# Kernel tuning notes

Hardware: AMD Instinct MI355X
Metric: run time of the kernel (lower is better)

The kernel has to match this reference:

```python
import jax, jax.numpy as jnp
import numpy as np

N = 100000      # nodes
E = 800000      # edges
F_IN = 256      # input feature dim
HID = 256       # hidden_channels
H = 8           # heads
C = HID // H    # per-head dim = 32
OUT = 128       # out_channels
EPS_BN = 1e-5
NEG_SLOPE = 0.2


def _segment_softmax(logits, seg, n):
    # logits: [E, H], softmax over edges sharing the same destination node
    m = jax.ops.segment_max(logits, seg, num_segments=n)          # [N, H]
    m = jnp.where(jnp.isfinite(m), m, 0.0)                         # nodes with no in-edges
    ex = jnp.exp(logits - m[seg])                                  # [E, H]
    denom = jax.ops.segment_sum(ex, seg, num_segments=n)          # [N, H]
    return ex / (denom[seg] + 1e-16)


def _gatv2_layer(x, src, dst, Wl, bl, Wr, br, att, bias):
    # PyG GATv2Conv (eval, concat=True): lin_l on source, lin_r on target
    n = x.shape[0]
    xl = (x @ Wl + bl).reshape(n, H, C)   # [N, H, C]
    xr = (x @ Wr + br).reshape(n, H, C)   # [N, H, C]
    e = jax.nn.leaky_relu(xl[src] + xr[dst], NEG_SLOPE)            # [E, H, C]
    logits = jnp.einsum('ehc,hc->eh', e, att)                      # [E, H]
    alpha = _segment_softmax(logits, dst, n)                       # [E, H]
    msg = xl[src] * alpha[:, :, None]                              # [E, H, C]
    out = jax.ops.segment_sum(msg, dst, num_segments=n)            # [N, H, C]
    return out.reshape(n, H * C) + bias


def _batchnorm(x, gamma, beta):
    # training-mode batch statistics (deterministic), biased variance
    mu = x.mean(axis=0)
    var = x.var(axis=0)
    return gamma * (x - mu) * jax.lax.rsqrt(var + EPS_BN) + beta


def setup_inputs() -> dict:
    key = jax.random.key(0)
    ks = jax.random.split(key, 12)
    s = 0.05
    z = jnp.zeros
    o = jnp.ones
    rn = lambda k, shp: jax.random.normal(k, shp, jnp.float32) * s
    return {
        'x': jax.random.normal(ks[0], (N, F_IN), jnp.float32),
        'edge_index': jax.random.randint(ks[1], (2, E), 0, N, jnp.int32),
        'Wl1': rn(ks[2], (F_IN, HID)), 'bl1': z((HID,), jnp.float32),
        'Wr1': rn(ks[3], (F_IN, HID)), 'br1': z((HID,), jnp.float32),
        'att1': rn(ks[4], (H, C)), 'bias1': z((HID,), jnp.float32),
        'gamma1': o((HID,), jnp.float32), 'beta1': z((HID,), jnp.float32),
        'Wl2': rn(ks[5], (HID, HID)), 'bl2': z((HID,), jnp.float32),
        'Wr2': rn(ks[6], (HID, HID)), 'br2': z((HID,), jnp.float32),
        'att2': rn(ks[7], (H, C)), 'bias2': z((HID,), jnp.float32),
        'gamma2': o((HID,), jnp.float32), 'beta2': z((HID,), jnp.float32),
        'Wfc': rn(ks[8], (HID, OUT)), 'bfc': z((OUT,), jnp.float32),
    }


def reference(x, edge_index, Wl1, bl1, Wr1, br1, att1, bias1, gamma1, beta1,
              Wl2, bl2, Wr2, br2, att2, bias2, gamma2, beta2, Wfc, bfc):
    src, dst = edge_index[0], edge_index[1]
    h = _gatv2_layer(x, src, dst, Wl1, bl1, Wr1, br1, att1, bias1)
    h = jax.nn.elu(_batchnorm(h, gamma1, beta1))
    h = _gatv2_layer(h, src, dst, Wl2, bl2, Wr2, br2, att2, bias2)
    h = jax.nn.elu(_batchnorm(h, gamma2, beta2))
    h = h @ Wfc + bfc
    # F.normalize(p=2, dim=-1)
    norm = jnp.maximum(jnp.linalg.norm(h, axis=-1, keepdims=True), 1e-12)
    return h / norm
```

## Files before the change

kernel.cpp:

```cpp
#include <hip/hip_runtime.h>
#include <math.h>

#define N_NODES 100000
#define N_EDGES 800000
#define NPAD    100096
#define FDIM 256
#define HEADS 8
#define CDIM 32
#define OUTF 128

#define SCAN_BLOCK 256
#define SCAN_NBLK ((N_NODES + SCAN_BLOCK - 1) / SCAN_BLOCK)

typedef _Float16 f16x2 __attribute__((ext_vector_type(2)));
typedef _Float16 f16x8 __attribute__((ext_vector_type(8)));
typedef float  f32x4 __attribute__((ext_vector_type(4)));
typedef unsigned short u16;

__device__ __forceinline__ u16 f2h(float f) {
    union { _Float16 h; u16 u; } c;
    c.h = (_Float16)f;
    return c.u;
}
__device__ __forceinline__ float h2f(u16 u) {
    union { u16 u; _Float16 h; } c;
    c.u = u;
    return (float)c.h;
}
__device__ __forceinline__ f16x2 u2h2(unsigned u) {
    return __builtin_bit_cast(f16x2, u);
}
__device__ __forceinline__ unsigned h2u2(f16x2 h) {
    return __builtin_bit_cast(unsigned, h);
}

__device__ __forceinline__ void gload_lds16(const void* g, void* l) {
    __builtin_amdgcn_global_load_lds((const __attribute__((address_space(1))) void*)g,
                                     (__attribute__((address_space(3))) void*)l, 16, 0, 0);
}

__global__ void cast_half(const float* __restrict__ src, int n_valid4, int n_pad4,
                          u16* __restrict__ dst) {
    int i = blockIdx.x * blockDim.x + threadIdx.x;
    int stride = gridDim.x * blockDim.x;
    for (; i < n_pad4; i += stride) {
        f32x4 v = {0.f, 0.f, 0.f, 0.f};
        if (i < n_valid4) v = ((const f32x4*)src)[i];
        ((ushort4*)dst)[i] = make_ushort4(f2h(v[0]), f2h(v[1]), f2h(v[2]), f2h(v[3]));
    }
}

__global__ void prep_w_layer(const float* __restrict__ Wl, const float* __restrict__ Wr,
                             u16* __restrict__ Wt) {
    int idx = blockIdx.x * blockDim.x + threadIdx.x;
    if (idx >= 512 * 256) return;
    int n = idx >> 8, k = idx & 255;
    float w = (n < 256) ? Wl[k * 256 + n] : Wr[k * 256 + (n - 256)];
    Wt[idx] = f2h(w);
}

__global__ void prep_w_fc(const float* __restrict__ Wfc, u16* __restrict__ Wt) {
    int idx = blockIdx.x * blockDim.x + threadIdx.x;
    if (idx >= 128 * 256) return;
    int n = idx >> 8, k = idx & 255;
    Wt[idx] = f2h(Wfc[k * 128 + n]);
}

template <bool HOUT, int NS, bool L2N>
__global__ __launch_bounds__(256) void gemm_h(
        const u16* __restrict__ A, const u16* __restrict__ Wt,
        const float* __restrict__ bias0, const float* __restrict__ bias1,
        void* __restrict__ C0v, void* __restrict__ C1v, int ldc, int M) {
    __shared__ __align__(16) u16 lA[2][128 * 64];
    __shared__ __align__(16) u16 lB[2][128 * 64];
    __shared__ float rssq[128];

    int tid = threadIdx.x;
    int wid = tid >> 6, lane = tid & 63;
    int wm = wid >> 1, wn = wid & 1;
    int lr = lane & 15, lk = lane >> 4;

    int orig = blockIdx.x;
    int nwg = gridDim.x;
    int q = nwg >> 3, r = nwg & 7;
    int xcd = orig & 7, loc = orig >> 3;
    int swz = (xcd < r) ? (xcd * (q + 1) + loc) : (r * (q + 1) + (xcd - r) * q + loc);
    int m0 = (swz / NS) * 128;
    int n0 = (swz % NS) * 128;

    auto stage = [&](int buf, int k0) {
#pragma unroll
        for (int i = 0; i < 4; i++) {
            int t = i * 256 + tid;
            int row = t >> 3;
            int ch = (t & 7) ^ (row & 7);
            gload_lds16(A + (size_t)(m0 + row) * 256 + k0 + ch * 8,
                        (char*)lA[buf] + i * 4096 + wid * 1024);
        }
#pragma unroll
        for (int i = 0; i < 4; i++) {
            int t = i * 256 + tid;
            int row = t >> 3;
            int ch = (t & 7) ^ (row & 7);
            gload_lds16(Wt + (size_t)(n0 + row) * 256 + k0 + ch * 8,
                        (char*)lB[buf] + i * 4096 + wid * 1024);
        }
    };

    f32x4 acc[4][4] = {};

    stage(0, 0);
    __syncthreads();

#pragma unroll 1
    for (int ks = 0; ks < 4; ks++) {
        int cur = ks & 1;
        if (ks < 3) stage(cur ^ 1, (ks + 1) * 64);

#pragma unroll
        for (int kk = 0; kk < 2; kk++) {
            f16x8 af[4], bf[4];
#pragma unroll
            for (int mr = 0; mr < 4; mr++) {
                int rr = wm * 64 + mr * 16 + lr;
                int qq = (kk * 4 + lk) ^ (rr & 7);
                af[mr] = *(const f16x8*)&lA[cur][rr * 64 + qq * 8];
            }
#pragma unroll
            for (int nr = 0; nr < 4; nr++) {
                int rr = wn * 64 + nr * 16 + lr;
                int qq = (kk * 4 + lk) ^ (rr & 7);
                bf[nr] = *(const f16x8*)&lB[cur][rr * 64 + qq * 8];
            }
#pragma unroll
            for (int mr = 0; mr < 4; mr++)
#pragma unroll
                for (int nr = 0; nr < 4; nr++)
                    acc[mr][nr] = __builtin_amdgcn_mfma_f32_16x16x32_f16(
                        af[mr], bf[nr], acc[mr][nr], 0, 0, 0);
        }
        __syncthreads();
    }

#pragma unroll
    for (int mr = 0; mr < 4; mr++)
#pragma unroll
        for (int nr = 0; nr < 4; nr++) {
            int col = n0 + wn * 64 + nr * 16 + lr;
            float b = (col < 256) ? bias0[col] : bias1[col - 256];
#pragma unroll
            for (int j = 0; j < 4; j++) acc[mr][nr][j] += b;
        }

    if constexpr (L2N) {
        if (tid < 128) rssq[tid] = 0.f;
        __syncthreads();
#pragma unroll
        for (int mr = 0; mr < 4; mr++)
#pragma unroll
            for (int j = 0; j < 4; j++) {
                int rl = wm * 64 + mr * 16 + lk * 4 + j;
                float s = 0.f;
#pragma unroll
                for (int nr = 0; nr < 4; nr++) s += acc[mr][nr][j] * acc[mr][nr][j];
                atomicAdd(&rssq[rl], s);
            }
        __syncthreads();
#pragma unroll
        for (int mr = 0; mr < 4; mr++)
#pragma unroll
            for (int j = 0; j < 4; j++) {
                int rl = wm * 64 + mr * 16 + lk * 4 + j;
                int row = m0 + rl;
                if (row < M) {
                    float inv = 1.f / fmaxf(sqrtf(rssq[rl]), 1e-12f);
#pragma unroll
                    for (int nr = 0; nr < 4; nr++) {
                        int col = n0 + wn * 64 + nr * 16 + lr;
                        ((float*)C0v)[(size_t)row * ldc + col] = acc[mr][nr][j] * inv;
                    }
                }
            }
    } else {
#pragma unroll
        for (int mr = 0; mr < 4; mr++)
#pragma unroll
            for (int nr = 0; nr < 4; nr++) {
                int col = n0 + wn * 64 + nr * 16 + lr;
                void* Cp; int c;
                if (col < 256) { Cp = C0v; c = col; }
                else           { Cp = C1v; c = col - 256; }
#pragma unroll
                for (int j = 0; j < 4; j++) {
                    int row = m0 + wm * 64 + mr * 16 + lk * 4 + j;
                    if (row < M) {
                        float v = acc[mr][nr][j];
                        if constexpr (HOUT)
                            ((u16*)Cp)[(size_t)row * ldc + c] = f2h(v);
                        else
                            ((float*)Cp)[(size_t)row * ldc + c] = v;
                    }
                }
            }
    }
}

__global__ void count_deg(const int* __restrict__ dstA, int* __restrict__ deg) {
    int i = blockIdx.x * blockDim.x + threadIdx.x;
    int stride = gridDim.x * blockDim.x;
    for (; i < N_EDGES; i += stride) atomicAdd(&deg[dstA[i]], 1);
}

__global__ void scan_phase1(const int* __restrict__ deg, int* __restrict__ blocksum) {
    __shared__ int sdata[SCAN_BLOCK];
    int i = blockIdx.x * SCAN_BLOCK + threadIdx.x;
    sdata[threadIdx.x] = (i < N_NODES) ? deg[i] : 0;
    __syncthreads();
    for (int off = SCAN_BLOCK / 2; off > 0; off >>= 1) {
        if (threadIdx.x < off) sdata[threadIdx.x] += sdata[threadIdx.x + off];
        __syncthreads();
    }
    if (threadIdx.x == 0) blocksum[blockIdx.x] = sdata[0];
}

__global__ void scan_phase2(int* __restrict__ blocksum) {
    __shared__ int part[512];
    int t = threadIdx.x;
    int v = (t < SCAN_NBLK) ? blocksum[t] : 0;
    part[t] = v;
    __syncthreads();
    for (int off = 1; off < 512; off <<= 1) {
        int u = 0;
        if (t >= off) u = part[t - off];
        __syncthreads();
        if (t >= off) part[t] += u;
        __syncthreads();
    }
    if (t < SCAN_NBLK) blocksum[t] = part[t] - v;
}

__global__ void scan_phase3(const int* __restrict__ deg, const int* __restrict__ blockoff,
                            int* __restrict__ rowstart, int* __restrict__ cursor) {
    __shared__ int part[SCAN_BLOCK];
    int t = threadIdx.x;
    int i = blockIdx.x * SCAN_BLOCK + t;
    int v = (i < N_NODES) ? deg[i] : 0;
    part[t] = v;
    __syncthreads();
    for (int off = 1; off < SCAN_BLOCK; off <<= 1) {
        int u = 0;
        if (t >= off) u = part[t - off];
        __syncthreads();
        if (t >= off) part[t] += u;
        __syncthreads();
    }
    if (i < N_NODES) {
        int excl = blockoff[blockIdx.x] + part[t] - v;
        rowstart[i] = excl;
        cursor[i] = excl;
        if (i == N_NODES - 1) rowstart[N_NODES] = blockoff[blockIdx.x] + part[t];
    }
}

__global__ void fill_csr(const int* __restrict__ srcA, const int* __restrict__ dstA,
                         int* __restrict__ cursor, int* __restrict__ csr_src) {
    int i = blockIdx.x * blockDim.x + threadIdx.x;
    int stride = gridDim.x * blockDim.x;
    for (; i < N_EDGES; i += stride) {
        int pos = atomicAdd(&cursor[dstA[i]], 1);
        csr_src[pos] = srcA[i];
    }
}

__global__ void gat_fused(const u16* __restrict__ xl, const u16* __restrict__ xr,
                          const int* __restrict__ rowstart, const int* __restrict__ csr_src,
                          const float* __restrict__ att, u16* __restrict__ out) {
    int wid = (blockIdx.x * blockDim.x + threadIdx.x) >> 6;
    int lane = threadIdx.x & 63;
    if (wid >= N_NODES) return;
    int hl = lane & 31;
    int up = lane >> 5;
    int c0 = hl * 8;

    uint4 xru = *(const uint4*)(xr + (size_t)wid * FDIM + c0);
    f16x2 xr0 = u2h2(xru.x), xr1 = u2h2(xru.y), xr2 = u2h2(xru.z), xr3 = u2h2(xru.w);
    f32x4 av0 = *(const f32x4*)(att + c0);
    f32x4 av1 = *(const f32x4*)(att + c0 + 4);
    f16x2 a0 = {(_Float16)av0[0], (_Float16)av0[1]};
    f16x2 a1 = {(_Float16)av0[2], (_Float16)av0[3]};
    f16x2 a2 = {(_Float16)av1[0], (_Float16)av1[1]};
    f16x2 a3 = {(_Float16)av1[2], (_Float16)av1[3]};
    const f16x2 k02 = {(_Float16)0.2f, (_Float16)0.2f};

    f16x2 acc0 = {(_Float16)0.f, (_Float16)0.f};
    f16x2 acc1 = acc0, acc2 = acc0, acc3 = acc0;
    float den = 0.f;

    int jb = rowstart[wid], je = rowstart[wid + 1];
    if (jb < je) {
        int jlast = je - 1;
        int nsteps = (je - jb + 1) >> 1;
        int i0 = jb + up;     if (i0 > jlast) i0 = jlast;
        uint4 u0 = *(const uint4*)(xl + (size_t)csr_src[i0] * FDIM + c0);
        int i1 = jb + 2 + up; if (i1 > jlast) i1 = jlast;
        uint4 u1 = *(const uint4*)(xl + (size_t)csr_src[i1] * FDIM + c0);
        int i2 = jb + 4 + up; if (i2 > jlast) i2 = jlast;
        uint4 u2 = *(const uint4*)(xl + (size_t)csr_src[i2] * FDIM + c0);

        for (int t = 0; t < nsteps; ++t) {
            int in_ = jb + 2 * t + 6 + up; if (in_ > jlast) in_ = jlast;
            uint4 un = *(const uint4*)(xl + (size_t)csr_src[in_] * FDIM + c0);

            int myidx = jb + 2 * t + up;
            f16x2 x0 = u2h2(u0.x), x1 = u2h2(u0.y), x2 = u2h2(u0.z), x3 = u2h2(u0.w);
            f16x2 v0 = x0 + xr0, v1 = x1 + xr1, v2 = x2 + xr2, v3 = x3 + xr3;
            f16x2 t0 = __builtin_elementwise_max(v0, v0 * k02);
            f16x2 t1 = __builtin_elementwise_max(v1, v1 * k02);
            f16x2 t2 = __builtin_elementwise_max(v2, v2 * k02);
            f16x2 t3 = __builtin_elementwise_max(v3, v3 * k02);
            float s = __builtin_amdgcn_fdot2(t0, a0, 0.f, false);
            s = __builtin_amdgcn_fdot2(t1, a1, s, false);
            s = __builtin_amdgcn_fdot2(t2, a2, s, false);
            s = __builtin_amdgcn_fdot2(t3, a3, s, false);
            s += __shfl_xor(s, 1);
            s += __shfl_xor(s, 2);
            float e = (myidx <= jlast) ? __expf(s) : 0.f;
            den += e;
            _Float16 eh = (_Float16)e;
            f16x2 ev = {eh, eh};
            acc0 += ev * x0;
            acc1 += ev * x1;
            acc2 += ev * x2;
            acc3 += ev * x3;
            u0 = u1; u1 = u2; u2 = un;
        }
    }
    den += __shfl_xor(den, 32);
    acc0 += u2h2(__shfl_xor((int)h2u2(acc0), 32));
    acc1 += u2h2(__shfl_xor((int)h2u2(acc1), 32));
    acc2 += u2h2(__shfl_xor((int)h2u2(acc2), 32));
    acc3 += u2h2(__shfl_xor((int)h2u2(acc3), 32));

    if (up == 0) {
        float invf = 1.f / (den + 1e-16f);
        u16 h[8];
        h[0] = f2h((float)acc0[0] * invf); h[1] = f2h((float)acc0[1] * invf);
        h[2] = f2h((float)acc1[0] * invf); h[3] = f2h((float)acc1[1] * invf);
        h[4] = f2h((float)acc2[0] * invf); h[5] = f2h((float)acc2[1] * invf);
        h[6] = f2h((float)acc3[0] * invf); h[7] = f2h((float)acc3[1] * invf);
        *(uint4*)(out + (size_t)wid * FDIM + c0) = *(const uint4*)h;
    }
}

__global__ void bn_stats_h(const u16* __restrict__ X, float* __restrict__ sum,
                           float* __restrict__ sumsq, int nrows) {
    int col = threadIdx.x;
    float s = 0.f, ss = 0.f;
    for (int r = blockIdx.x; r < nrows; r += gridDim.x) {
        float v = h2f(X[(size_t)r * FDIM + col]);
        s += v;
        ss += v * v;
    }
    atomicAdd(&sum[col], s);
    atomicAdd(&sumsq[col], ss);
}

__global__ void bn_finalize(const float* __restrict__ sum, const float* __restrict__ sumsq,
                            const float* __restrict__ gamma, const float* __restrict__ beta,
                            float* __restrict__ scale, float* __restrict__ shift) {
    int c = threadIdx.x;
    float mean = sum[c] * (1.f / N_NODES);
    float var = sumsq[c] * (1.f / N_NODES) - mean * mean;
    float sc = gamma[c] * rsqrtf(var + 1e-5f);
    scale[c] = sc;
    shift[c] = beta[c] - mean * sc;
}

__global__ void bn_elu_h(const u16* __restrict__ X, const float* __restrict__ scale,
                         const float* __restrict__ shift, u16* __restrict__ dst) {
    int i = blockIdx.x * blockDim.x + threadIdx.x;
    int stride = gridDim.x * blockDim.x;
    const int n_valid4 = N_NODES * FDIM / 4;
    const int n_pad4 = NPAD * FDIM / 4;
    for (; i < n_pad4; i += stride) {
        u16 h[4] = {0, 0, 0, 0};
        if (i < n_valid4) {
            ushort4 v = ((const ushort4*)X)[i];
            int c0 = (i * 4) & (FDIM - 1);
            float f0 = h2f(v.x) * scale[c0 + 0] + shift[c0 + 0];
            float f1 = h2f(v.y) * scale[c0 + 1] + shift[c0 + 1];
            float f2 = h2f(v.z) * scale[c0 + 2] + shift[c0 + 2];
            float f3 = h2f(v.w) * scale[c0 + 3] + shift[c0 + 3];
            f0 = f0 > 0.f ? f0 : expf(f0) - 1.f;
            f1 = f1 > 0.f ? f1 : expf(f1) - 1.f;
            f2 = f2 > 0.f ? f2 : expf(f2) - 1.f;
            f3 = f3 > 0.f ? f3 : expf(f3) - 1.f;
            h[0] = f2h(f0); h[1] = f2h(f1); h[2] = f2h(f2); h[3] = f2h(f3);
        }
        ((ushort4*)dst)[i] = make_ushort4(h[0], h[1], h[2], h[3]);
    }
}

extern "C" void kernel_launch(void* const* d_in, const int* in_sizes, int n_in,
                              void* d_out, int out_size, void* d_ws, size_t ws_size,
                              hipStream_t stream) {
    const float* x     = (const float*)d_in[0];
    const int*   ei    = (const int*)d_in[1];
    const float* Wl1   = (const float*)d_in[2];
    const float* bl1   = (const float*)d_in[3];
    const float* Wr1   = (const float*)d_in[4];
    const float* br1   = (const float*)d_in[5];
    const float* att1  = (const float*)d_in[6];
    const float* gamma1 = (const float*)d_in[8];
    const float* beta1  = (const float*)d_in[9];
    const float* Wl2   = (const float*)d_in[10];
    const float* bl2   = (const float*)d_in[11];
    const float* Wr2   = (const float*)d_in[12];
    const float* br2   = (const float*)d_in[13];
    const float* att2  = (const float*)d_in[14];
    const float* gamma2 = (const float*)d_in[16];
    const float* beta2  = (const float*)d_in[17];
    const float* Wfc   = (const float*)d_in[18];
    const float* bfc   = (const float*)d_in[19];

    const int* srcA = ei;
    const int* dstA = ei + N_EDGES;

    const size_t REG = (size_t)NPAD * FDIM * 4;
    char* p = (char*)d_ws;
    char* R0 = p;            p += REG;
    char* R1 = p;            p += REG;
    char* R2 = p;            p += REG;
    u16* WTH   = (u16*)p;              p += 512 * 256 * 2;
    float* SUM = (float*)p;            p += FDIM * 4;
    float* SQ  = (float*)p;            p += FDIM * 4;
    float* SC  = (float*)p;            p += FDIM * 4;
    float* SH  = (float*)p;            p += FDIM * 4;
    int* DEG      = (int*)p;           p += (size_t)N_NODES * 4;
    int* ROWSTART = (int*)p;           p += (size_t)(N_NODES + 1) * 4;
    int* CURSOR   = (int*)p;           p += (size_t)N_NODES * 4;
    int* CSR      = (int*)p;           p += (size_t)N_EDGES * 4;
    int* BLKSUM   = (int*)p;           p += (size_t)SCAN_NBLK * 4;

    const int gat_grid = (N_NODES + 3) / 4;
    const int gemm_grid_layer = (NPAD / 128) * 4;
    const int gemm_grid_fc = NPAD / 128;

    hipMemsetAsync(DEG, 0, (size_t)N_NODES * sizeof(int), stream);
    count_deg<<<2048, 256, 0, stream>>>(dstA, DEG);
    scan_phase1<<<SCAN_NBLK, SCAN_BLOCK, 0, stream>>>(DEG, BLKSUM);
    scan_phase2<<<1, 512, 0, stream>>>(BLKSUM);
    scan_phase3<<<SCAN_NBLK, SCAN_BLOCK, 0, stream>>>(DEG, BLKSUM, ROWSTART, CURSOR);
    fill_csr<<<2048, 256, 0, stream>>>(srcA, dstA, CURSOR, CSR);

    cast_half<<<4096, 256, 0, stream>>>(x, N_NODES * FDIM / 4, NPAD * FDIM / 4, (u16*)R0);
    prep_w_layer<<<512, 256, 0, stream>>>(Wl1, Wr1, WTH);
    gemm_h<true, 4, false><<<gemm_grid_layer, 256, 0, stream>>>((u16*)R0, WTH, bl1, br1, R1, R2, 256, N_NODES);
    gat_fused<<<gat_grid, 256, 0, stream>>>((u16*)R1, (u16*)R2, ROWSTART, CSR, att1, (u16*)R0);

    hipMemsetAsync(SUM, 0, 2 * FDIM * sizeof(float), stream);
    bn_stats_h<<<1024, 256, 0, stream>>>((u16*)R0, SUM, SQ, N_NODES);
    bn_finalize<<<1, 256, 0, stream>>>(SUM, SQ, gamma1, beta1, SC, SH);
    bn_elu_h<<<2048, 256, 0, stream>>>((u16*)R0, SC, SH, (u16*)R1);

    prep_w_layer<<<512, 256, 0, stream>>>(Wl2, Wr2, WTH);
    gemm_h<true, 4, false><<<gemm_grid_layer, 256, 0, stream>>>((u16*)R1, WTH, bl2, br2, R2, R0, 256, N_NODES);
    gat_fused<<<gat_grid, 256, 0, stream>>>((u16*)R2, (u16*)R0, ROWSTART, CSR, att2, (u16*)R1);

    hipMemsetAsync(SUM, 0, 2 * FDIM * sizeof(float), stream);
    bn_stats_h<<<1024, 256, 0, stream>>>((u16*)R1, SUM, SQ, N_NODES);
    bn_finalize<<<1, 256, 0, stream>>>(SUM, SQ, gamma2, beta2, SC, SH);
    bn_elu_h<<<2048, 256, 0, stream>>>((u16*)R1, SC, SH, (u16*)R2);

    prep_w_fc<<<128, 256, 0, stream>>>(Wfc, WTH);
    gemm_h<false, 1, true><<<gemm_grid_fc, 256, 0, stream>>>((u16*)R2, WTH, bfc, bfc, d_out, d_out, 128, N_NODES);
}
```

Baseline: 631.8 us.

## Widen GEMM to 8 waves, batch GAT gathers by 8, vectorize BN stats

The GEMM kernel now runs 512 threads per block. Each wave computes a 32x64 sub-tile instead of 64x64, which roughly halves the accumulator registers per thread and puts more waves on each CU. The GAT aggregation loop now handles 8 edges per iteration and issues four gathered row loads ahead of time per lane pair, instead of a rolling 3-deep prefetch, to keep more memory requests in flight. bn_stats reads 4 halves per thread, reduces across the block in shared memory and issues fewer atomics. The costs are more clamped redundant loads for low-degree nodes and a larger block-level sync footprint in the GEMM.

```diff
diff --git a/kernel.cpp b/kernel.cpp
--- a/kernel.cpp
+++ b/kernel.cpp
@@ -67,7 +67,7 @@
 }
 
 template <bool HOUT, int NS, bool L2N>
-__global__ __launch_bounds__(256) void gemm_h(
+__global__ __launch_bounds__(512) void gemm_h(
         const u16* __restrict__ A, const u16* __restrict__ Wt,
         const float* __restrict__ bias0, const float* __restrict__ bias1,
         void* __restrict__ C0v, void* __restrict__ C1v, int ldc, int M) {
@@ -90,24 +90,24 @@
 
     auto stage = [&](int buf, int k0) {
 #pragma unroll
-        for (int i = 0; i < 4; i++) {
-            int t = i * 256 + tid;
+        for (int i = 0; i < 2; i++) {
+            int t = i * 512 + tid;
             int row = t >> 3;
             int ch = (t & 7) ^ (row & 7);
             gload_lds16(A + (size_t)(m0 + row) * 256 + k0 + ch * 8,
-                        (char*)lA[buf] + i * 4096 + wid * 1024);
-        }
-#pragma unroll
-        for (int i = 0; i < 4; i++) {
-            int t = i * 256 + tid;
+                        (char*)lA[buf] + i * 8192 + wid * 1024);
+        }
+#pragma unroll
+        for (int i = 0; i < 2; i++) {
+            int t = i * 512 + tid;
             int row = t >> 3;
             int ch = (t & 7) ^ (row & 7);
             gload_lds16(Wt + (size_t)(n0 + row) * 256 + k0 + ch * 8,
-                        (char*)lB[buf] + i * 4096 + wid * 1024);
+                        (char*)lB[buf] + i * 8192 + wid * 1024);
         }
     };
 
-    f32x4 acc[4][4] = {};
+    f32x4 acc[2][4] = {};
 
     stage(0, 0);
     __syncthreads();
@@ -119,10 +119,10 @@
 
 #pragma unroll
         for (int kk = 0; kk < 2; kk++) {
-            f16x8 af[4], bf[4];
-#pragma unroll
-            for (int mr = 0; mr < 4; mr++) {
-                int rr = wm * 64 + mr * 16 + lr;
+            f16x8 af[2], bf[4];
+#pragma unroll
+            for (int mr = 0; mr < 2; mr++) {
+                int rr = wm * 32 + mr * 16 + lr;
                 int qq = (kk * 4 + lk) ^ (rr & 7);
                 af[mr] = *(const f16x8*)&lA[cur][rr * 64 + qq * 8];
             }
@@ -133,7 +133,7 @@
                 bf[nr] = *(const f16x8*)&lB[cur][rr * 64 + qq * 8];
             }
 #pragma unroll
-            for (int mr = 0; mr < 4; mr++)
+            for (int mr = 0; mr < 2; mr++)
 #pragma unroll
                 for (int nr = 0; nr < 4; nr++)
                     acc[mr][nr] = __builtin_amdgcn_mfma_f32_16x16x32_f16(
@@ -143,7 +143,7 @@
     }
 
 #pragma unroll
-    for (int mr = 0; mr < 4; mr++)
+    for (int mr = 0; mr < 2; mr++)
 #pragma unroll
         for (int nr = 0; nr < 4; nr++) {
             int col = n0 + wn * 64 + nr * 16 + lr;
@@ -156,10 +156,10 @@
         if (tid < 128) rssq[tid] = 0.f;
         __syncthreads();
 #pragma unroll
-        for (int mr = 0; mr < 4; mr++)
+        for (int mr = 0; mr < 2; mr++)
 #pragma unroll
             for (int j = 0; j < 4; j++) {
-                int rl = wm * 64 + mr * 16 + lk * 4 + j;
+                int rl = wm * 32 + mr * 16 + lk * 4 + j;
                 float s = 0.f;
 #pragma unroll
                 for (int nr = 0; nr < 4; nr++) s += acc[mr][nr][j] * acc[mr][nr][j];
@@ -167,10 +167,10 @@
             }
         __syncthreads();
 #pragma unroll
-        for (int mr = 0; mr < 4; mr++)
+        for (int mr = 0; mr < 2; mr++)
 #pragma unroll
             for (int j = 0; j < 4; j++) {
-                int rl = wm * 64 + mr * 16 + lk * 4 + j;
+                int rl = wm * 32 + mr * 16 + lk * 4 + j;
                 int row = m0 + rl;
                 if (row < M) {
                     float inv = 1.f / fmaxf(sqrtf(rssq[rl]), 1e-12f);
@@ -183,7 +183,7 @@
             }
     } else {
 #pragma unroll
-        for (int mr = 0; mr < 4; mr++)
+        for (int mr = 0; mr < 2; mr++)
 #pragma unroll
             for (int nr = 0; nr < 4; nr++) {
                 int col = n0 + wn * 64 + nr * 16 + lr;
@@ -192,7 +192,7 @@
                 else           { Cp = C1v; c = col - 256; }
 #pragma unroll
                 for (int j = 0; j < 4; j++) {
-                    int row = m0 + wm * 64 + mr * 16 + lk * 4 + j;
+                    int row = m0 + wm * 32 + mr * 16 + lk * 4 + j;
                     if (row < M) {
                         float v = acc[mr][nr][j];
                         if constexpr (HOUT)
@@ -299,40 +299,47 @@
     int jb = rowstart[wid], je = rowstart[wid + 1];
     if (jb < je) {
         int jlast = je - 1;
-        int nsteps = (je - jb + 1) >> 1;
-        int i0 = jb + up;     if (i0 > jlast) i0 = jlast;
-        uint4 u0 = *(const uint4*)(xl + (size_t)csr_src[i0] * FDIM + c0);
-        int i1 = jb + 2 + up; if (i1 > jlast) i1 = jlast;
-        uint4 u1 = *(const uint4*)(xl + (size_t)csr_src[i1] * FDIM + c0);
-        int i2 = jb + 4 + up; if (i2 > jlast) i2 = jlast;
-        uint4 u2 = *(const uint4*)(xl + (size_t)csr_src[i2] * FDIM + c0);
+        int D = je - jb;
+        int nsteps = (D + 7) >> 3;
+        auto clamp = [&](int e) { return e > jlast ? jlast : e; };
+
+        uint4 u[4], n[4];
+#pragma unroll
+        for (int k = 0; k < 4; k++)
+            u[k] = *(const uint4*)(xl + (size_t)csr_src[clamp(jb + up + 2 * k)] * FDIM + c0);
 
         for (int t = 0; t < nsteps; ++t) {
-            int in_ = jb + 2 * t + 6 + up; if (in_ > jlast) in_ = jlast;
-            uint4 un = *(const uint4*)(xl + (size_t)csr_src[in_] * FDIM + c0);
-
-            int myidx = jb + 2 * t + up;
-            f16x2 x0 = u2h2(u0.x), x1 = u2h2(u0.y), x2 = u2h2(u0.z), x3 = u2h2(u0.w);
-            f16x2 v0 = x0 + xr0, v1 = x1 + xr1, v2 = x2 + xr2, v3 = x3 + xr3;
-            f16x2 t0 = __builtin_elementwise_max(v0, v0 * k02);
-            f16x2 t1 = __builtin_elementwise_max(v1, v1 * k02);
-            f16x2 t2 = __builtin_elementwise_max(v2, v2 * k02);
-            f16x2 t3 = __builtin_elementwise_max(v3, v3 * k02);
-            float s = __builtin_amdgcn_fdot2(t0, a0, 0.f, false);
-            s = __builtin_amdgcn_fdot2(t1, a1, s, false);
-            s = __builtin_amdgcn_fdot2(t2, a2, s, false);
-            s = __builtin_amdgcn_fdot2(t3, a3, s, false);
-            s += __shfl_xor(s, 1);
-            s += __shfl_xor(s, 2);
-            float e = (myidx <= jlast) ? __expf(s) : 0.f;
-            den += e;
-            _Float16 eh = (_Float16)e;
-            f16x2 ev = {eh, eh};
-            acc0 += ev * x0;
-            acc1 += ev * x1;
-            acc2 += ev * x2;
-            acc3 += ev * x3;
-            u0 = u1; u1 = u2; u2 = un;
+            int base = jb + 8 * t + up;
+#pragma unroll
+            for (int k = 0; k < 4; k++)
+                n[k] = *(const uint4*)(xl + (size_t)csr_src[clamp(base + 8 + 2 * k)] * FDIM + c0);
+
+#pragma unroll
+            for (int k = 0; k < 4; k++) {
+                f16x2 x0 = u2h2(u[k].x), x1 = u2h2(u[k].y);
+                f16x2 x2 = u2h2(u[k].z), x3 = u2h2(u[k].w);
+                f16x2 v0 = x0 + xr0, v1 = x1 + xr1, v2 = x2 + xr2, v3 = x3 + xr3;
+                f16x2 t0 = __builtin_elementwise_max(v0, v0 * k02);
+                f16x2 t1 = __builtin_elementwise_max(v1, v1 * k02);
+                f16x2 t2 = __builtin_elementwise_max(v2, v2 * k02);
+                f16x2 t3 = __builtin_elementwise_max(v3, v3 * k02);
+                float s = __builtin_amdgcn_fdot2(t0, a0, 0.f, false);
+                s = __builtin_amdgcn_fdot2(t1, a1, s, false);
+                s = __builtin_amdgcn_fdot2(t2, a2, s, false);
+                s = __builtin_amdgcn_fdot2(t3, a3, s, false);
+                s += __shfl_xor(s, 1);
+                s += __shfl_xor(s, 2);
+                float e = (base + 2 * k <= jlast) ? __expf(s) : 0.f;
+                den += e;
+                _Float16 eh = (_Float16)e;
+                f16x2 ev = {eh, eh};
+                acc0 += ev * x0;
+                acc1 += ev * x1;
+                acc2 += ev * x2;
+                acc3 += ev * x3;
+            }
+#pragma unroll
+            for (int k = 0; k < 4; k++) u[k] = n[k];
         }
     }
     den += __shfl_xor(den, 32);
@@ -354,15 +361,32 @@
 
 __global__ void bn_stats_h(const u16* __restrict__ X, float* __restrict__ sum,
                            float* __restrict__ sumsq, int nrows) {
-    int col = threadIdx.x;
-    float s = 0.f, ss = 0.f;
-    for (int r = blockIdx.x; r < nrows; r += gridDim.x) {
-        float v = h2f(X[(size_t)r * FDIM + col]);
-        s += v;
-        ss += v * v;
-    }
-    atomicAdd(&sum[col], s);
-    atomicAdd(&sumsq[col], ss);
+    __shared__ float red[4][64][8];
+    int tid = threadIdx.x;
+    int cg = tid & 63;
+    int rg = tid >> 6;
+    float s0 = 0.f, s1 = 0.f, s2 = 0.f, s3 = 0.f;
+    float q0 = 0.f, q1 = 0.f, q2 = 0.f, q3 = 0.f;
+    for (int r = blockIdx.x * 4 + rg; r < nrows; r += gridDim.x * 4) {
+        ushort4 v = *(const ushort4*)&X[(size_t)r * FDIM + cg * 4];
+        float f0 = h2f(v.x), f1 = h2f(v.y), f2 = h2f(v.z), f3 = h2f(v.w);
+        s0 += f0; q0 += f0 * f0;
+        s1 += f1; q1 += f1 * f1;
+        s2 += f2; q2 += f2 * f2;
+        s3 += f3; q3 += f3 * f3;
+    }
+    red[rg][cg][0] = s0; red[rg][cg][1] = s1; red[rg][cg][2] = s2; red[rg][cg][3] = s3;
+    red[rg][cg][4] = q0; red[rg][cg][5] = q1; red[rg][cg][6] = q2; red[rg][cg][7] = q3;
+    __syncthreads();
+    if (tid < 64) {
+#pragma unroll
+        for (int i = 0; i < 4; i++) {
+            float ts = red[0][tid][i] + red[1][tid][i] + red[2][tid][i] + red[3][tid][i];
+            atomicAdd(&sum[tid * 4 + i], ts);
+            float tq = red[0][tid][4 + i] + red[1][tid][4 + i] + red[2][tid][4 + i] + red[3][tid][4 + i];
+            atomicAdd(&sumsq[tid * 4 + i], tq);
+        }
+    }
 }
 
 __global__ void bn_finalize(const float* __restrict__ sum, const float* __restrict__ sumsq,
@@ -455,7 +479,7 @@
 
     cast_half<<<4096, 256, 0, stream>>>(x, N_NODES * FDIM / 4, NPAD * FDIM / 4, (u16*)R0);
     prep_w_layer<<<512, 256, 0, stream>>>(Wl1, Wr1, WTH);
-    gemm_h<true, 4, false><<<gemm_grid_layer, 256, 0, stream>>>((u16*)R0, WTH, bl1, br1, R1, R2, 256, N_NODES);
+    gemm_h<true, 4, false><<<gemm_grid_layer, 512, 0, stream>>>((u16*)R0, WTH, bl1, br1, R1, R2, 256, N_NODES);
     gat_fused<<<gat_grid, 256, 0, stream>>>((u16*)R1, (u16*)R2, ROWSTART, CSR, att1, (u16*)R0);
 
     hipMemsetAsync(SUM, 0, 2 * FDIM * sizeof(float), stream);
@@ -464,7 +488,7 @@
     bn_elu_h<<<2048, 256, 0, stream>>>((u16*)R0, SC, SH, (u16*)R1);
 
     prep_w_layer<<<512, 256, 0, stream>>>(Wl2, Wr2, WTH);
-    gemm_h<true, 4, false><<<gemm_grid_layer, 256, 0, stream>>>((u16*)R1, WTH, bl2, br2, R2, R0, 256, N_NODES);
+    gemm_h<true, 4, false><<<gemm_grid_layer, 512, 0, stream>>>((u16*)R1, WTH, bl2, br2, R2, R0, 256, N_NODES);
     gat_fused<<<gat_grid, 256, 0, stream>>>((u16*)R2, (u16*)R0, ROWSTART, CSR, att2, (u16*)R1);
 
     hipMemsetAsync(SUM, 0, 2 * FDIM * sizeof(float), stream);
@@ -473,5 +497,5 @@
     bn_elu_h<<<2048, 256, 0, stream>>>((u16*)R1, SC, SH, (u16*)R2);
 
     prep_w_fc<<<128, 256, 0, stream>>>(Wfc, WTH);
-    gemm_h<false, 1, true><<<gemm_grid_fc, 256, 0, stream>>>((u16*)R2, WTH, bfc, bfc, d_out, d_out, 128, N_NODES);
-}
+    gemm_h<false, 1, true><<<gemm_grid_fc, 512, 0, stream>>>((u16*)R2, WTH, bfc, bfc, d_out, d_out, 128, N_NODES);
+}
```

Result: slower. 703.4 us (+11.3%).
